# Optimization experiments

Measured on AMD Instinct MI355X. Metric: run time of the kernel, lower is better.

## Reference

```python
import jax, jax.numpy as jnp
import numpy as np

N_NODES = 50000
N_EDGES = 800000
DIM_IN = 128
DIM_OUT = 64
HEADS = 4
NEG_SLOPE = 0.2


def setup_inputs() -> dict:
    key = jax.random.key(0)
    k_x, k_e, k_w, k_a = jax.random.split(key, 4)
    x = jax.random.normal(k_x, (N_NODES, DIM_IN), dtype=jnp.float32)
    edge_index = jax.random.randint(k_e, (2, N_EDGES), 0, N_NODES, dtype=jnp.int32)
    # Stacked per-head params: W (Linear(dim_in, dim_out, bias=False)) and
    # a (Linear(2*dim_out, 1, bias=False)) for each of HEADS heads.
    W = jax.random.normal(k_w, (HEADS, DIM_IN, DIM_OUT), dtype=jnp.float32) * (1.0 / np.sqrt(DIM_IN))
    a = jax.random.normal(k_a, (HEADS, 2 * DIM_OUT), dtype=jnp.float32) * (1.0 / np.sqrt(2 * DIM_OUT))
    return {"x": x, "edge_index": edge_index, "W": W, "a": a}


def _gat_forward(x, W, a, edge_index):
    src = edge_index[0]  # segment for softmax / scatter target
    dst = edge_index[1]  # node whose features are gathered (x_j)
    # h: [N, H, D]
    h = jnp.einsum('nd,hdo->nho', x, W)
    a_i = a[:, :DIM_OUT]   # [H, D] applied to x_i
    a_j = a[:, DIM_OUT:]   # [H, D] applied to x_j
    # per-node attention logit halves: [N, H]
    s_i = jnp.einsum('nhd,hd->nh', h, a_i)
    s_j = jnp.einsum('nhd,hd->nh', h, a_j)
    e = jax.nn.leaky_relu(s_i[src] + s_j[dst], NEG_SLOPE)  # [E, H]
    # segment softmax over edges grouped by src node
    m = jax.ops.segment_max(e, src, num_segments=N_NODES)  # [N, H]
    ex = jnp.exp(e - m[src])
    denom = jax.ops.segment_sum(ex, src, num_segments=N_NODES)  # [N, H]
    att = ex / denom[src]  # [E, H]
    # weighted scatter-sum of gathered features: [N, H, D]
    msgs = att[:, :, None] * h[dst]
    h_prime = jax.ops.segment_sum(msgs, src, num_segments=N_NODES)
    # concat=False -> mean over heads
    return jnp.mean(h_prime, axis=1)  # [N, D]


def reference(x, edge_index, W, a):
    return _gat_forward(x, W, a, edge_index)
```

## Files before the change

### kernel.cpp

```cpp
#include <hip/hip_runtime.h>
#include <hip/hip_bf16.h>

#define N_NODES 50000
#define N_EDGES 800000
#define DIM_IN  128
#define DIM_OUT 64
#define HEADS   4
#define NEG_SLOPE 0.2f
#define NPB 32
#define GEMM_BLOCKS ((N_NODES + NPB - 1) / NPB)
#define N_PAD (GEMM_BLOCKS * NPB)
#define PAD 64

__device__ __forceinline__ unsigned int f2bf(float f) {
    unsigned int u = __float_as_uint(f);
    return (u + 0x7FFFu + ((u >> 16) & 1u)) >> 16;
}
__device__ __forceinline__ float bf2f(unsigned int b) {
    return __uint_as_float(b << 16);
}
__device__ __forceinline__ float4 f4fma(float s, float4 w, float4 c) {
    c.x = fmaf(s, w.x, c.x); c.y = fmaf(s, w.y, c.y);
    c.z = fmaf(s, w.z, c.z); c.w = fmaf(s, w.w, c.w);
    return c;
}

__global__ __launch_bounds__(256) void fat_kernel(
    const float* __restrict__ x, const float* __restrict__ W,
    const float* __restrict__ a,
    unsigned short* __restrict__ h2, float* __restrict__ s_i, float* __restrict__ s_j,
    const int* __restrict__ ei, int* __restrict__ cursor, unsigned short* __restrict__ sdst)
{
    __shared__ __align__(16) unsigned char smem[NPB * DIM_IN * 4];
    const int b = blockIdx.x;
    const int t = threadIdx.x;

    if (b % 3 != 0) {
        const int s = (b / 3) * 2 + (b % 3 - 1);
        const int e = s * 256 + t;
        if (e < N_EDGES) {
            const int src = ei[e];
            const int r = atomicAdd(&cursor[src], 1);
            if (r < PAD) sdst[src * PAD + r] = (unsigned short)ei[N_EDGES + e];
        }
        return;
    }

    float4 (*xs)[DIM_IN / 4] = (float4 (*)[DIM_IN / 4])smem;
    const int nb = (b / 3) * NPB;
    {
        const float4* xg = (const float4*)x;
        const int base = nb * (DIM_IN / 4);
        const int limit = N_NODES * (DIM_IN / 4);
#pragma unroll
        for (int r = 0; r < 4; ++r) {
            const int idx = t + 256 * r;
            const int g = base + idx;
            float4 v = {0.f, 0.f, 0.f, 0.f};
            if (g < limit) v = xg[g];
            ((float4*)&xs[0][0])[idx] = v;
        }
    }
    __syncthreads();

    const int nslot = t >> 6;
    const int head  = (t >> 4) & 3;
    const int oq    = t & 15;

    const float4* Wv = (const float4*)(W + head * (DIM_IN * DIM_OUT)) + oq;
    float4 acc[8];
#pragma unroll
    for (int k = 0; k < 8; ++k) acc[k] = make_float4(0.f, 0.f, 0.f, 0.f);

#pragma unroll 2
    for (int d4 = 0; d4 < DIM_IN / 4; ++d4) {
        const float4 w0 = Wv[(4 * d4 + 0) * 16];
        const float4 w1 = Wv[(4 * d4 + 1) * 16];
        const float4 w2 = Wv[(4 * d4 + 2) * 16];
        const float4 w3 = Wv[(4 * d4 + 3) * 16];
#pragma unroll
        for (int k = 0; k < 8; ++k) {
            const float4 xv = xs[nslot + 4 * k][d4];
            acc[k] = f4fma(xv.w, w3, f4fma(xv.z, w2, f4fma(xv.y, w1, f4fma(xv.x, w0, acc[k]))));
        }
    }
    __syncthreads();

    unsigned short* lt16 = (unsigned short*)smem;
#pragma unroll
    for (int k = 0; k < 8; ++k) {
        const int base = (nslot + 4 * k) * (DIM_OUT * HEADS) + oq * 16 + head;
        lt16[base + 0]  = (unsigned short)f2bf(acc[k].x);
        lt16[base + 4]  = (unsigned short)f2bf(acc[k].y);
        lt16[base + 8]  = (unsigned short)f2bf(acc[k].z);
        lt16[base + 12] = (unsigned short)f2bf(acc[k].w);
    }

    const float4 ai = *(const float4*)(a + head * (2 * DIM_OUT) + oq * 4);
    const float4 aj = *(const float4*)(a + head * (2 * DIM_OUT) + DIM_OUT + oq * 4);
#pragma unroll
    for (int k = 0; k < 8; ++k) {
        const int n = nb + nslot + 4 * k;
        float pi = acc[k].x * ai.x + acc[k].y * ai.y + acc[k].z * ai.z + acc[k].w * ai.w;
        float pj = acc[k].x * aj.x + acc[k].y * aj.y + acc[k].z * aj.z + acc[k].w * aj.w;
#pragma unroll
        for (int off = 8; off > 0; off >>= 1) {
            pi += __shfl_down(pi, off, 16);
            pj += __shfl_down(pj, off, 16);
        }
        if (oq == 0) {
            s_i[n * HEADS + head] = pi;
            s_j[n * HEADS + head] = pj;
        }
    }
    __syncthreads();

    const uint4* lt4 = (const uint4*)smem;
    uint4* hg = (uint4*)(h2 + (size_t)nb * (DIM_OUT * HEADS));
#pragma unroll
    for (int r = 0; r < 4; ++r) {
        const int idx = t + 256 * r;
        hg[idx] = lt4[idx];
    }
}

__global__ __launch_bounds__(256) void fused_kernel(
    const int* __restrict__ cursor, const unsigned short* __restrict__ sdst,
    const float* __restrict__ s_i, const float* __restrict__ s_j,
    const unsigned short* __restrict__ h2, float* __restrict__ out)
{
    __shared__ float4 att_s[4][64];
    __shared__ int    dst_s[4][64];
    const int wid = (blockIdx.x * 256 + threadIdx.x) >> 6;
    const int w = (threadIdx.x >> 6) & 3;
    const int lane = threadIdx.x & 63;
    if (wid >= N_NODES) return;
    const int n = wid;
    const int d = min(cursor[n], PAD);
    const int start = n * PAD;

    float acc = 0.f;
    if (d > 0) {
        const float4 si = *(const float4*)(s_i + n * HEADS);
        float4 m4 = {-INFINITY, -INFINITY, -INFINITY, -INFINITY};
        float4 cz = {-INFINITY, -INFINITY, -INFINITY, -INFINITY};
        int cdst = 0;
        if (lane < d) {
            cdst = (int)sdst[start + lane];
            const float4 sj = *(const float4*)(s_j + cdst * HEADS);
            float z0 = si.x + sj.x, z1 = si.y + sj.y, z2 = si.z + sj.z, z3 = si.w + sj.w;
            cz.x = z0 >= 0.f ? z0 : NEG_SLOPE * z0;
            cz.y = z1 >= 0.f ? z1 : NEG_SLOPE * z1;
            cz.z = z2 >= 0.f ? z2 : NEG_SLOPE * z2;
            cz.w = z3 >= 0.f ? z3 : NEG_SLOPE * z3;
            m4 = cz;
        }
#pragma unroll
        for (int off = 32; off > 0; off >>= 1) {
            m4.x = fmaxf(m4.x, __shfl_xor(m4.x, off, 64));
            m4.y = fmaxf(m4.y, __shfl_xor(m4.y, off, 64));
            m4.z = fmaxf(m4.z, __shfl_xor(m4.z, off, 64));
            m4.w = fmaxf(m4.w, __shfl_xor(m4.w, off, 64));
        }
        float4 ex = {0.f, 0.f, 0.f, 0.f};
        if (lane < d) {
            ex.x = __expf(cz.x - m4.x);
            ex.y = __expf(cz.y - m4.y);
            ex.z = __expf(cz.z - m4.z);
            ex.w = __expf(cz.w - m4.w);
        }
        float4 sm = ex;
#pragma unroll
        for (int off = 32; off > 0; off >>= 1) {
            sm.x += __shfl_xor(sm.x, off, 64);
            sm.y += __shfl_xor(sm.y, off, 64);
            sm.z += __shfl_xor(sm.z, off, 64);
            sm.w += __shfl_xor(sm.w, off, 64);
        }
        if (lane < d) {
            att_s[w][lane] = make_float4(ex.x / sm.x, ex.y / sm.y, ex.z / sm.z, ex.w / sm.w);
            dst_s[w][lane] = cdst;
        }
        for (int e = 0; e < d; ++e) {
            const float4 a4 = att_s[w][e];
            const int dd = dst_s[w][e];
            const uint2 hv = *(const uint2*)(h2 + (size_t)dd * (DIM_OUT * HEADS) + lane * HEADS);
            acc += a4.x * bf2f(hv.x & 0xFFFFu) + a4.y * bf2f(hv.x >> 16)
                 + a4.z * bf2f(hv.y & 0xFFFFu) + a4.w * bf2f(hv.y >> 16);
        }
    }
    out[n * DIM_OUT + lane] = 0.25f * acc;
}

extern "C" void kernel_launch(void* const* d_in, const int* in_sizes, int n_in,
                              void* d_out, int out_size, void* d_ws, size_t ws_size,
                              hipStream_t stream) {
    const float* x  = (const float*)d_in[0];
    const int*   ei = (const int*)d_in[1];
    const float* W  = (const float*)d_in[2];
    const float* a  = (const float*)d_in[3];
    float* out = (float*)d_out;

    char* ws = (char*)d_ws;
    size_t off = 0;
    auto alloc = [&](size_t bytes) { void* p = ws + off; off = (off + bytes + 511) & ~size_t(511); return p; };
    unsigned short* h2 = (unsigned short*)alloc(sizeof(unsigned short) * N_PAD * DIM_OUT * HEADS);
    float* s_i    = (float*)alloc(sizeof(float) * N_PAD * HEADS);
    float* s_j    = (float*)alloc(sizeof(float) * N_PAD * HEADS);
    int*   cursor = (int*)alloc(sizeof(int) * N_NODES);
    unsigned short* sdst = (unsigned short*)alloc(sizeof(unsigned short) * N_NODES * PAD);

    hipMemsetAsync(cursor, 0, sizeof(int) * N_NODES, stream);

    fat_kernel<<<3 * GEMM_BLOCKS, 256, 0, stream>>>(x, W, a, h2, s_i, s_j, ei, cursor, sdst);

    const int fb = (N_NODES * 64 + 255) / 256;
    fused_kernel<<<fb, 256, 0, stream>>>(cursor, sdst, s_i, s_j, h2, out);
}
```

Baseline: 203.0 us.

## Batch edge scatter per thread and unroll gather loop for memory-level parallelism

The scatter part of the fat kernel now has each thread load 16 edges with int4 reads and issue their atomics together, in place of one edge per thread interleaved with the GEMM blocks. The GEMM blocks now come first in the grid and the scatter blocks follow them. In the aggregation kernel the per-edge gather loop is unrolled by 8 and then 4, so several h2 row loads are in flight before their FMAs run. The intent is to hide global-memory latency and cut block and launch overhead in the scatter. The cost is more registers per thread and fewer threads available for the scatter phase.

```diff
diff --git a/kernel.cpp b/kernel.cpp
--- a/kernel.cpp
+++ b/kernel.cpp
@@ -11,6 +11,10 @@
 #define GEMM_BLOCKS ((N_NODES + NPB - 1) / NPB)
 #define N_PAD (GEMM_BLOCKS * NPB)
 #define PAD 64
+#define EPT 16
+#define SCAT_THREADS (N_EDGES / EPT)
+#define SCAT_BLOCKS ((SCAT_THREADS + 255) / 256)
+#define FAT_GRID (GEMM_BLOCKS + SCAT_BLOCKS)
 
 __device__ __forceinline__ unsigned int f2bf(float f) {
     unsigned int u = __float_as_uint(f);
@@ -35,19 +39,33 @@
     const int b = blockIdx.x;
     const int t = threadIdx.x;
 
-    if (b % 3 != 0) {
-        const int s = (b / 3) * 2 + (b % 3 - 1);
-        const int e = s * 256 + t;
-        if (e < N_EDGES) {
-            const int src = ei[e];
-            const int r = atomicAdd(&cursor[src], 1);
-            if (r < PAD) sdst[src * PAD + r] = (unsigned short)ei[N_EDGES + e];
+    if (b >= GEMM_BLOCKS) {
+        const int i = (b - GEMM_BLOCKS) * 256 + t;
+        if (i < SCAT_THREADS) {
+            const int e0 = i * EPT;
+            int4 s4[4], d4v[4];
+#pragma unroll
+            for (int q = 0; q < 4; ++q) {
+                s4[q]  = *(const int4*)(ei + e0 + 4 * q);
+                d4v[q] = *(const int4*)(ei + N_EDGES + e0 + 4 * q);
+            }
+#pragma unroll
+            for (int q = 0; q < 4; ++q) {
+                const int r0 = atomicAdd(&cursor[s4[q].x], 1);
+                const int r1 = atomicAdd(&cursor[s4[q].y], 1);
+                const int r2 = atomicAdd(&cursor[s4[q].z], 1);
+                const int r3 = atomicAdd(&cursor[s4[q].w], 1);
+                if (r0 < PAD) sdst[s4[q].x * PAD + r0] = (unsigned short)d4v[q].x;
+                if (r1 < PAD) sdst[s4[q].y * PAD + r1] = (unsigned short)d4v[q].y;
+                if (r2 < PAD) sdst[s4[q].z * PAD + r2] = (unsigned short)d4v[q].z;
+                if (r3 < PAD) sdst[s4[q].w * PAD + r3] = (unsigned short)d4v[q].w;
+            }
         }
         return;
     }
 
     float4 (*xs)[DIM_IN / 4] = (float4 (*)[DIM_IN / 4])smem;
-    const int nb = (b / 3) * NPB;
+    const int nb = b * NPB;
     {
         const float4* xg = (const float4*)x;
         const int base = nb * (DIM_IN / 4);
@@ -55,9 +73,9 @@
 #pragma unroll
         for (int r = 0; r < 4; ++r) {
             const int idx = t + 256 * r;
-            const int g = base + idx;
+            const int gi = base + idx;
             float4 v = {0.f, 0.f, 0.f, 0.f};
-            if (g < limit) v = xg[g];
+            if (gi < limit) v = xg[gi];
             ((float4*)&xs[0][0])[idx] = v;
         }
     }
@@ -181,10 +199,43 @@
             att_s[w][lane] = make_float4(ex.x / sm.x, ex.y / sm.y, ex.z / sm.z, ex.w / sm.w);
             dst_s[w][lane] = cdst;
         }
-        for (int e = 0; e < d; ++e) {
+
+        const unsigned short* hbase = h2 + lane * HEADS;
+        int e = 0;
+        for (; e + 8 <= d; e += 8) {
+            uint2 hv[8];
+            float4 at[8];
+#pragma unroll
+            for (int q = 0; q < 8; ++q) {
+                const int dd = dst_s[w][e + q];
+                at[q] = att_s[w][e + q];
+                hv[q] = *(const uint2*)(hbase + (size_t)dd * (DIM_OUT * HEADS));
+            }
+#pragma unroll
+            for (int q = 0; q < 8; ++q) {
+                acc += at[q].x * bf2f(hv[q].x & 0xFFFFu) + at[q].y * bf2f(hv[q].x >> 16)
+                     + at[q].z * bf2f(hv[q].y & 0xFFFFu) + at[q].w * bf2f(hv[q].y >> 16);
+            }
+        }
+        for (; e + 4 <= d; e += 4) {
+            uint2 hv[4];
+            float4 at[4];
+#pragma unroll
+            for (int q = 0; q < 4; ++q) {
+                const int dd = dst_s[w][e + q];
+                at[q] = att_s[w][e + q];
+                hv[q] = *(const uint2*)(hbase + (size_t)dd * (DIM_OUT * HEADS));
+            }
+#pragma unroll
+            for (int q = 0; q < 4; ++q) {
+                acc += at[q].x * bf2f(hv[q].x & 0xFFFFu) + at[q].y * bf2f(hv[q].x >> 16)
+                     + at[q].z * bf2f(hv[q].y & 0xFFFFu) + at[q].w * bf2f(hv[q].y >> 16);
+            }
+        }
+        for (; e < d; ++e) {
+            const int dd = dst_s[w][e];
             const float4 a4 = att_s[w][e];
-            const int dd = dst_s[w][e];
-            const uint2 hv = *(const uint2*)(h2 + (size_t)dd * (DIM_OUT * HEADS) + lane * HEADS);
+            const uint2 hv = *(const uint2*)(hbase + (size_t)dd * (DIM_OUT * HEADS));
             acc += a4.x * bf2f(hv.x & 0xFFFFu) + a4.y * bf2f(hv.x >> 16)
                  + a4.z * bf2f(hv.y & 0xFFFFu) + a4.w * bf2f(hv.y >> 16);
         }
@@ -212,7 +263,7 @@
 
     hipMemsetAsync(cursor, 0, sizeof(int) * N_NODES, stream);
 
-    fat_kernel<<<3 * GEMM_BLOCKS, 256, 0, stream>>>(x, W, a, h2, s_i, s_j, ei, cursor, sdst);
+    fat_kernel<<<FAT_GRID, 256, 0, stream>>>(x, W, a, h2, s_i, s_j, ei, cursor, sdst);
 
     const int fb = (N_NODES * 64 + 255) / 256;
     fused_kernel<<<fb, 256, 0, stream>>>(cursor, sdst, s_i, s_j, h2, out);
```

New measurement: 211.1 us. 1.04x slower.
